# Optimization experiments

Measured on AMD Instinct MI355X. Metric: run time of the kernel, lower is better.

Reference implementation:

```python
import jax, jax.numpy as jnp
import numpy as np

B, NQ, NKV = 4, 1024, 2048
Q_DIM = K_DIM = V_DIM = 1024
HEADS, DIM_HEAD = 16, 64
INNER = HEADS * DIM_HEAD


def setup_inputs() -> dict:
    key = jax.random.key(0)
    ks = jax.random.split(key, 10)
    return {
        "x": jax.random.normal(ks[0], (B, NQ, Q_DIM), dtype=jnp.float32),
        "key_t": jax.random.normal(ks[1], (B, NKV, K_DIM), dtype=jnp.float32),
        "value": jax.random.normal(ks[2], (B, NKV, V_DIM), dtype=jnp.float32),
        "mask": jax.random.randint(ks[3], (B, NQ, NKV), 0, 2) == 1,
        "Wq": jax.random.normal(ks[4], (Q_DIM, INNER), dtype=jnp.float32) * (Q_DIM ** -0.5),
        "Wk": jax.random.normal(ks[5], (K_DIM, INNER), dtype=jnp.float32) * (K_DIM ** -0.5),
        "Wv": jax.random.normal(ks[6], (V_DIM, INNER), dtype=jnp.float32) * (V_DIM ** -0.5),
        "Wo": jax.random.normal(ks[7], (INNER, Q_DIM), dtype=jnp.float32) * (INNER ** -0.5),
        "gamma": jnp.ones((Q_DIM,), dtype=jnp.float32),
        "beta": jnp.zeros((Q_DIM,), dtype=jnp.float32),
    }


def reference(x, key_t, value, mask, Wq, Wk, Wv, Wo, gamma, beta):
    # LayerNorm over last dim
    mu = jnp.mean(x, axis=-1, keepdims=True)
    var = jnp.var(x, axis=-1, keepdims=True)
    xn = (x - mu) * jax.lax.rsqrt(var + 1e-5) * gamma + beta

    h, d = HEADS, DIM_HEAD
    # b n (h d) -> b h n d
    q = (xn @ Wq).reshape(B, NQ, h, d).transpose(0, 2, 1, 3)
    k = (key_t @ Wk).reshape(B, NKV, h, d).transpose(0, 2, 1, 3)
    v = (value @ Wv).reshape(B, NKV, h, d).transpose(0, 2, 1, 3)

    scale = d ** -0.5
    dots = jnp.einsum("bhnd,bhmd->bhnm", q, k) * scale  # [b,h,nq,nkv]
    min_neg = -jnp.finfo(dots.dtype).max
    dots = jnp.where(mask[:, None, :, :], min_neg, dots)
    attn = jax.nn.softmax(dots, axis=-1)
    out = jnp.einsum("bhnm,bhmd->bhnd", attn, v)
    out = out.transpose(0, 2, 1, 3).reshape(B, NQ, INNER)  # b h n d -> b n (h d)
    return out @ Wo
```

## Files before the change

### kernel.cpp

```cpp
#include <hip/hip_runtime.h>

typedef unsigned short u16;
typedef unsigned int u32;
typedef unsigned char u8;
typedef unsigned long long u64;

typedef __attribute__((ext_vector_type(8))) short bf16x8;
typedef __attribute__((ext_vector_type(4))) short bf16x4;
typedef __attribute__((ext_vector_type(4))) float f32x4;

__device__ __forceinline__ float bf2f(u16 u) {
    union { u32 i; float f; } v; v.i = ((u32)u) << 16; return v.f;
}
__device__ __forceinline__ u16 f2bf(float f) {
    union { float f; u32 i; } v; v.f = f;
    u32 r = v.i + 0x7fffu + ((v.i >> 16) & 1u);
    return (u16)(r >> 16);
}
__device__ __forceinline__ u32 pkbf(float a, float b) {
    return (u32)f2bf(a) | ((u32)f2bf(b) << 16);
}
__device__ __forceinline__ float fexp2(float x) { return __builtin_amdgcn_exp2f(x); }

__device__ __forceinline__ void async16(u16* lds, const u16* g) {
    __builtin_amdgcn_global_load_lds(
        (const __attribute__((address_space(1))) void*)g,
        (__attribute__((address_space(3))) void*)lds, 16, 0, 0);
}

__global__ __launch_bounds__(256) void detect_dtype(const u32* __restrict__ x,
                                                    int* __restrict__ flag) {
    int tid = threadIdx.x;
    int hits = 0;
    for (int i = 0; i < 4; ++i) {
        u32 w = x[tid * 4 + i];
        u32 e = (w >> 7) & 0xFFu;
        hits += (e >= 110u && e <= 131u) ? 1 : 0;
    }
    for (int off = 1; off < 64; off <<= 1) hits += __shfl_xor(hits, off, 64);
    __shared__ int red[4];
    int wave = tid >> 6, lane = tid & 63;
    if (lane == 0) red[wave] = hits;
    __syncthreads();
    if (tid == 0) flag[0] = (red[0] + red[1] + red[2] + red[3] > 512) ? 1 : 0;
}

__global__ __launch_bounds__(256) void conv_bf16_2(const void* __restrict__ src0,
                                                   const void* __restrict__ src1,
                                                   u16* __restrict__ dst0,
                                                   u16* __restrict__ dst1,
                                                   const int* __restrict__ flagp,
                                                   int half_blocks) {
    int flag = *flagp;
    const void* src = (blockIdx.x < (u32)half_blocks) ? src0 : src1;
    u16* dst = (blockIdx.x < (u32)half_blocks) ? dst0 : dst1;
    int blk = (blockIdx.x < (u32)half_blocks) ? blockIdx.x : (blockIdx.x - half_blocks);
    size_t i = (size_t)blk * 256 + threadIdx.x;
    if (flag) {
        ((uint4*)dst)[i] = ((const uint4*)src)[i];
    } else {
        const float4* s = (const float4*)src + i * 2;
        float4 f0 = s[0], f1 = s[1];
        u16 t[8];
        t[0] = f2bf(f0.x); t[1] = f2bf(f0.y); t[2] = f2bf(f0.z); t[3] = f2bf(f0.w);
        t[4] = f2bf(f1.x); t[5] = f2bf(f1.y); t[6] = f2bf(f1.z); t[7] = f2bf(f1.w);
        ((uint4*)dst)[i] = *(const uint4*)t;
    }
}

__global__ __launch_bounds__(256) void mask_bits(const int* __restrict__ m,
                                                 u64* __restrict__ o) {
    int wid  = (blockIdx.x * 256 + threadIdx.x) >> 6;
    int lane = threadIdx.x & 63;
    size_t base = (size_t)wid * 2048;
    for (int it = 0; it < 8; ++it) {
        u64 b0 = __ballot(m[base + it * 256 +   0 + lane] == 0);
        u64 b1 = __ballot(m[base + it * 256 +  64 + lane] == 0);
        u64 b2 = __ballot(m[base + it * 256 + 128 + lane] == 0);
        u64 b3 = __ballot(m[base + it * 256 + 192 + lane] == 0);
        if (lane == 0) {
            size_t idx = (base + it * 256) >> 6;
            o[idx + 0] = b0; o[idx + 1] = b1; o[idx + 2] = b2; o[idx + 3] = b3;
        }
    }
}

__global__ __launch_bounds__(256) void ln_kernel(const void* __restrict__ x_,
                                                 const void* __restrict__ g_,
                                                 const void* __restrict__ b_,
                                                 u16* __restrict__ out,
                                                 const int* __restrict__ flagp) {
    int flag = *flagp;
    int row = blockIdx.x;
    int tid = threadIdx.x;
    float v[4];
    if (flag) {
        const u16* xr = (const u16*)x_ + (size_t)row * 1024;
        uint2 d = *(const uint2*)&xr[tid * 4];
        v[0] = bf2f((u16)(d.x & 0xffff));
        v[1] = bf2f((u16)(d.x >> 16));
        v[2] = bf2f((u16)(d.y & 0xffff));
        v[3] = bf2f((u16)(d.y >> 16));
    } else {
        const float* xr = (const float*)x_ + (size_t)row * 1024;
        float4 d = *(const float4*)&xr[tid * 4];
        v[0] = d.x; v[1] = d.y; v[2] = d.z; v[3] = d.w;
    }
    float s  = v[0] + v[1] + v[2] + v[3];
    float ss = v[0]*v[0] + v[1]*v[1] + v[2]*v[2] + v[3]*v[3];
    for (int off = 1; off < 64; off <<= 1) {
        s  += __shfl_xor(s,  off, 64);
        ss += __shfl_xor(ss, off, 64);
    }
    __shared__ float red[8];
    int wave = tid >> 6, lane = tid & 63;
    if (lane == 0) { red[wave] = s; red[4 + wave] = ss; }
    __syncthreads();
    s  = red[0] + red[1] + red[2] + red[3];
    ss = red[4] + red[5] + red[6] + red[7];
    float mu   = s * (1.0f / 1024.0f);
    float var  = ss * (1.0f / 1024.0f) - mu * mu;
    float rstd = rsqrtf(var + 1e-5f);
    u16 r01[4];
    for (int j = 0; j < 4; ++j) {
        float g, bb;
        if (flag) { g = bf2f(((const u16*)g_)[tid * 4 + j]); bb = bf2f(((const u16*)b_)[tid * 4 + j]); }
        else      { g = ((const float*)g_)[tid * 4 + j];     bb = ((const float*)b_)[tid * 4 + j]; }
        r01[j] = f2bf((v[j] - mu) * rstd * g + bb);
    }
    uint2 o;
    o.x = (u32)r01[0] | ((u32)r01[1] << 16);
    o.y = (u32)r01[2] | ((u32)r01[3] << 16);
    *(uint2*)&out[(size_t)row * 1024 + tid * 4] = o;
}

__global__ __launch_bounds__(256) void transpose64x4(const void* __restrict__ s0,
                                                     const void* __restrict__ s1,
                                                     const void* __restrict__ s2,
                                                     const void* __restrict__ s3,
                                                     u16* __restrict__ d0,
                                                     u16* __restrict__ d1,
                                                     u16* __restrict__ d2,
                                                     u16* __restrict__ d3,
                                                     int rows, int cols,
                                                     const int* __restrict__ flagp) {
    __shared__ u16 t[64][65];
    int flag = *flagp;
    const void* src_ = (blockIdx.z == 0) ? s0 : (blockIdx.z == 1) ? s1 :
                       (blockIdx.z == 2) ? s2 : s3;
    u16* dst = (blockIdx.z == 0) ? d0 : (blockIdx.z == 1) ? d1 :
               (blockIdx.z == 2) ? d2 : d3;
    int bx = blockIdx.x * 64;
    int by = blockIdx.y * 64;
    int tid = threadIdx.x;
    for (int i = 0; i < 16; ++i) {
        int r = i * 4 + (tid >> 6);
        int c = tid & 63;
        size_t idx = (size_t)(by + r) * cols + bx + c;
        t[r][c] = flag ? ((const u16*)src_)[idx] : f2bf(((const float*)src_)[idx]);
    }
    __syncthreads();
    for (int i = 0; i < 16; ++i) {
        int r = i * 4 + (tid >> 6);
        int c = tid & 63;
        dst[(size_t)(bx + r) * rows + by + c] = t[c][r];
    }
}

__global__ __launch_bounds__(256, 3) void gemm128(const u16* __restrict__ A,
                                                  const u16* __restrict__ Bt,
                                                  void* __restrict__ C_,
                                                  int M, int N, int K,
                                                  const int* __restrict__ flagp,
                                                  int c_flagged, float cscale,
                                                  int vt_mode, int mdiv) {
    __shared__ u16 As[128 * 64];
    __shared__ u16 Bs[128 * 64];
    int flag = *flagp;
    bool c_bf16 = c_flagged ? (flag != 0) : true;

    int id  = blockIdx.x;
    int j   = id >> 3;
    int gy  = (id & 7) + 8 * (j % mdiv);
    int bnt = j / mdiv;

    int tid  = threadIdx.x;
    int wave = tid >> 6, lane = tid & 63;
    int quad = lane >> 4, l16 = lane & 15;
    size_t bm = (size_t)gy * 128;
    size_t bn = (size_t)bnt * 128;
    int wm = (wave >> 1) * 64, wn = (wave & 1) * 64;

    int lr  = lane >> 3;
    int csw = (lane & 7) ^ lr;
    const u16* Ag = A  + (bm + wave * 32 + lr) * (size_t)K + csw * 8;
    const u16* Bg = Bt + (bn + wave * 32 + lr) * (size_t)K + csw * 8;
    u16* Al = &As[(wave * 32) * 64];
    u16* Bl = &Bs[(wave * 32) * 64];

    f32x4 acc[4][4];
#pragma unroll
    for (int i = 0; i < 4; ++i)
#pragma unroll
        for (int jj = 0; jj < 4; ++jj)
            acc[i][jj] = (f32x4){0.f, 0.f, 0.f, 0.f};

    int rsw = l16 & 7;

    for (int k0 = 0; k0 < K; k0 += 64) {
        __syncthreads();
#pragma unroll
        for (int i = 0; i < 4; ++i) {
            async16(Al + i * 8 * 64, Ag + (size_t)i * 8 * K + k0);
            async16(Bl + i * 8 * 64, Bg + (size_t)i * 8 * K + k0);
        }
        __syncthreads();

#pragma unroll
        for (int ks = 0; ks < 2; ++ks) {
            int chunk = ((ks << 2) | quad) ^ rsw;
            bf16x8 af[4], bfr[4];
#pragma unroll
            for (int mi = 0; mi < 4; ++mi)
                af[mi]  = *(const bf16x8*)&As[(wm + mi * 16 + l16) * 64 + chunk * 8];
#pragma unroll
            for (int ni = 0; ni < 4; ++ni)
                bfr[ni] = *(const bf16x8*)&Bs[(wn + ni * 16 + l16) * 64 + chunk * 8];
#pragma unroll
            for (int mi = 0; mi < 4; ++mi)
#pragma unroll
                for (int ni = 0; ni < 4; ++ni)
                    acc[mi][ni] = __builtin_amdgcn_mfma_f32_16x16x32_bf16(
                        af[mi], bfr[ni], acc[mi][ni], 0, 0, 0);
        }
    }

    if (vt_mode) {
        u16* C = (u16*)C_;
#pragma unroll
        for (int mi = 0; mi < 4; ++mi)
#pragma unroll
            for (int ni = 0; ni < 4; ++ni) {
                size_t m = bm + wm + mi * 16 + quad * 4;
                size_t n = bn + wn + ni * 16 + l16;
                size_t bb = m >> 11, kv = m & 2047;
                size_t hh = n >> 6,  d  = n & 63;
                u16 t4[4];
#pragma unroll
                for (int r = 0; r < 4; ++r) t4[r] = f2bf(acc[mi][ni][r]);
                *(uint2*)&C[((bb * 16 + hh) * 64 + d) * 2048 + kv] = *(const uint2*)t4;
            }
    } else {
#pragma unroll
        for (int mi = 0; mi < 4; ++mi)
#pragma unroll
            for (int ni = 0; ni < 4; ++ni)
#pragma unroll
                for (int r = 0; r < 4; ++r) {
                    size_t row = bm + wm + mi * 16 + quad * 4 + r;
                    size_t col = bn + wn + ni * 16 + l16;
                    float val = acc[mi][ni][r] * cscale;
                    if (c_bf16) ((u16*)C_)[row * N + col]   = f2bf(val);
                    else        ((float*)C_)[row * N + col] = val;
                }
    }
}

__global__ __launch_bounds__(256, 3) void gemm128_vk(const u16* __restrict__ A0,
                                                     const u16* __restrict__ Bt0,
                                                     u16* __restrict__ C0,
                                                     const u16* __restrict__ A1,
                                                     const u16* __restrict__ Bt1,
                                                     u16* __restrict__ C1) {
    __shared__ u16 As[128 * 64];
    __shared__ u16 Bs[128 * 64];
    const int N = 1024, K = 1024, mdiv = 8;

    int id  = blockIdx.x;
    int seg = id >> 9;
    int lid = id & 511;
    const u16* A  = seg ? A1 : A0;
    const u16* Bt = seg ? Bt1 : Bt0;

    int j   = lid >> 3;
    int gy  = (lid & 7) + 8 * (j % mdiv);
    int bnt = j / mdiv;

    int tid  = threadIdx.x;
    int wave = tid >> 6, lane = tid & 63;
    int quad = lane >> 4, l16 = lane & 15;
    size_t bm = (size_t)gy * 128;
    size_t bn = (size_t)bnt * 128;
    int wm = (wave >> 1) * 64, wn = (wave & 1) * 64;

    int lr  = lane >> 3;
    int csw = (lane & 7) ^ lr;
    const u16* Ag = A  + (bm + wave * 32 + lr) * (size_t)K + csw * 8;
    const u16* Bg = Bt + (bn + wave * 32 + lr) * (size_t)K + csw * 8;
    u16* Al = &As[(wave * 32) * 64];
    u16* Bl = &Bs[(wave * 32) * 64];

    f32x4 acc[4][4];
#pragma unroll
    for (int i = 0; i < 4; ++i)
#pragma unroll
        for (int jj = 0; jj < 4; ++jj)
            acc[i][jj] = (f32x4){0.f, 0.f, 0.f, 0.f};

    int rsw = l16 & 7;

    for (int k0 = 0; k0 < K; k0 += 64) {
        __syncthreads();
#pragma unroll
        for (int i = 0; i < 4; ++i) {
            async16(Al + i * 8 * 64, Ag + (size_t)i * 8 * K + k0);
            async16(Bl + i * 8 * 64, Bg + (size_t)i * 8 * K + k0);
        }
        __syncthreads();

#pragma unroll
        for (int ks = 0; ks < 2; ++ks) {
            int chunk = ((ks << 2) | quad) ^ rsw;
            bf16x8 af[4], bfr[4];
#pragma unroll
            for (int mi = 0; mi < 4; ++mi)
                af[mi]  = *(const bf16x8*)&As[(wm + mi * 16 + l16) * 64 + chunk * 8];
#pragma unroll
            for (int ni = 0; ni < 4; ++ni)
                bfr[ni] = *(const bf16x8*)&Bs[(wn + ni * 16 + l16) * 64 + chunk * 8];
#pragma unroll
            for (int mi = 0; mi < 4; ++mi)
#pragma unroll
                for (int ni = 0; ni < 4; ++ni)
                    acc[mi][ni] = __builtin_amdgcn_mfma_f32_16x16x32_bf16(
                        af[mi], bfr[ni], acc[mi][ni], 0, 0, 0);
        }
    }

    if (!seg) {
        u16* C = C0;
#pragma unroll
        for (int mi = 0; mi < 4; ++mi)
#pragma unroll
            for (int ni = 0; ni < 4; ++ni) {
                size_t m = bm + wm + mi * 16 + quad * 4;
                size_t n = bn + wn + ni * 16 + l16;
                size_t bb = m >> 11, kv = m & 2047;
                size_t hh = n >> 6,  d  = n & 63;
                u16 t4[4];
#pragma unroll
                for (int r = 0; r < 4; ++r) t4[r] = f2bf(acc[mi][ni][r]);
                *(uint2*)&C[((bb * 16 + hh) * 64 + d) * 2048 + kv] = *(const uint2*)t4;
            }
    } else {
        u16* C = C1;
#pragma unroll
        for (int mi = 0; mi < 4; ++mi)
#pragma unroll
            for (int ni = 0; ni < 4; ++ni)
#pragma unroll
                for (int r = 0; r < 4; ++r) {
                    size_t row = bm + wm + mi * 16 + quad * 4 + r;
                    size_t col = bn + wn + ni * 16 + l16;
                    C[row * N + col] = f2bf(acc[mi][ni][r]);
                }
    }
}

__global__ __launch_bounds__(256) void attn_kernel(const u16* __restrict__ qg,
                                                   const u16* __restrict__ kg,
                                                   const u16* __restrict__ vtg,
                                                   const u32* __restrict__ mbits,
                                                   float* __restrict__ o0,
                                                   float* __restrict__ o1b0,
                                                   float* __restrict__ o1b1,
                                                   float* __restrict__ o1b2,
                                                   float* __restrict__ o1b3,
                                                   float* __restrict__ lacc0,
                                                   float* __restrict__ lacc1) {
    __shared__ u16 Ks[64 * 64];
    __shared__ u16 Vst[64 * 64];

    const int NQc = 1024, NKVc = 2048, HD = 1024;
    int id = blockIdx.x;
    int j  = id >> 3;
    int qt2 = j >> 3;
    int half = qt2 >> 4;
    int qt = qt2 & 15;
    int g  = (id & 7) + ((j & 7) << 3);
    int h  = g & 15;
    int b  = g >> 4;

    int tid  = threadIdx.x;
    int wave = tid >> 6, lane = tid & 63;
    int quad = lane >> 4, l16 = lane & 15;
    int q0 = qt * 64;

    const u16* qrow = qg + ((size_t)b * NQc + q0 + wave * 16 + l16) * HD + h * 64;
    bf16x8 aq0 = *(const bf16x8*)&qrow[quad * 8];
    bf16x8 aq1 = *(const bf16x8*)&qrow[32 + quad * 8];

    int lr  = lane >> 3;
    int csw = (lane & 7) ^ lr;
    const u16* kbase = kg  + ((size_t)b * NKVc + wave * 8 + lr) * HD + h * 64 + csw * 8;
    const u16* vbase = vtg + (((size_t)b * 16 + h) * 64 + wave * 8 + lr) * (size_t)NKVc + csw * 8;
    u16* kl = Ks  + (wave * 8) * 64;
    u16* vl = Vst + (wave * 8) * 64;

    f32x4 O[4], lacc;
#pragma unroll
    for (int dt = 0; dt < 4; ++dt) O[dt] = (f32x4){0.f, 0.f, 0.f, 0.f};
    lacc = (f32x4){0.f, 0.f, 0.f, 0.f};

    bf16x4 ones4;
#pragma unroll
    for (int jj = 0; jj < 4; ++jj) ones4[jj] = (short)0x3F80;

    const u32* mrowb = mbits + ((size_t)b * NQc + q0 + wave * 16 + l16) * 64;

    int l7 = l16 & 7;
    int kvbeg = half << 10;

    for (int kv0 = kvbeg; kv0 < kvbeg + 1024; kv0 += 64) {
        __syncthreads();
#pragma unroll
        for (int i = 0; i < 2; ++i) {
            async16(kl + i * 32 * 64, kbase + ((size_t)kv0 + i * 32) * HD);
            async16(vl + i * 32 * 64, vbase + (size_t)(i * 32) * NKVc + kv0);
        }
        __syncthreads();

        uint2 bw = *(const uint2*)&mrowb[kv0 >> 5];

        bf16x4 pfr[4];
#pragma unroll
        for (int nt = 0; nt < 4; ++nt) {
            const u16* krow = Ks + (nt * 16 + l16) * 64;
            bf16x8 bk0 = *(const bf16x8*)&krow[(quad ^ l7) * 8];
            bf16x8 bk1 = *(const bf16x8*)&krow[((4 + quad) ^ l7) * 8];
            f32x4 st = (f32x4){0.f, 0.f, 0.f, 0.f};
            st = __builtin_amdgcn_mfma_f32_16x16x32_bf16(bk0, aq0, st, 0, 0, 0);
            st = __builtin_amdgcn_mfma_f32_16x16x32_bf16(bk1, aq1, st, 0, 0, 0);

            u32 w  = (nt < 2) ? bw.x : bw.y;
            u32 m4 = (w >> (((nt & 1) << 4) + (quad << 2))) & 0xFu;
            u32 m01 = ((m4 & 1u) ? 0xFFFFu : 0u) | ((m4 & 2u) ? 0xFFFF0000u : 0u);
            u32 m23 = ((m4 & 4u) ? 0xFFFFu : 0u) | ((m4 & 8u) ? 0xFFFF0000u : 0u);
            u32 p01 = pkbf(fexp2(st[0]), fexp2(st[1])) & m01;
            u32 p23 = pkbf(fexp2(st[2]), fexp2(st[3])) & m23;
            uint2 pu; pu.x = p01; pu.y = p23;
            pfr[nt] = *(const bf16x4*)&pu;

            lacc = __builtin_amdgcn_mfma_f32_16x16x16bf16_1k(ones4, pfr[nt], lacc, 0, 0, 0);
        }

#pragma unroll
        for (int dt = 0; dt < 4; ++dt) {
            const u16* vrow = Vst + (dt * 16 + l16) * 64;
#pragma unroll
            for (int kvs = 0; kvs < 4; ++kvs) {
                int gran = ((kvs << 1) | (quad >> 1)) ^ l7;
                bf16x4 av = *(const bf16x4*)&vrow[gran * 8 + (quad & 1) * 4];
                O[dt] = __builtin_amdgcn_mfma_f32_16x16x16bf16_1k(av, pfr[kvs], O[dt], 0, 0, 0);
            }
        }
    }

    int qi = q0 + wave * 16 + l16;
    float* opart = half ? (b == 0 ? o1b0 : b == 1 ? o1b1 : b == 2 ? o1b2 : o1b3) : o0;
    size_t rbase = half ? (size_t)qi : ((size_t)b * NQc + qi);
    float* orow = opart + rbase * 1024 + h * 64;
#pragma unroll
    for (int dt = 0; dt < 4; ++dt)
        *(float4*)&orow[dt * 16 + quad * 4] = (float4){O[dt][0], O[dt][1], O[dt][2], O[dt][3]};

    float* lp = half ? lacc1 : lacc0;
    if (quad == 0) lp[((size_t)b * 16 + h) * 1024 + qi] = lacc[0];
}

__global__ __launch_bounds__(256) void combine_halves(const float* __restrict__ p0,
                                                      const float* __restrict__ p1b0,
                                                      const float* __restrict__ p1b1,
                                                      const float* __restrict__ p1b2,
                                                      const float* __restrict__ p1b3,
                                                      const float* __restrict__ l0,
                                                      const float* __restrict__ l1,
                                                      u16* __restrict__ ao) {
    int row = blockIdx.x;
    int b = row >> 10, qq = row & 1023;
    const float* p1 = (b == 0) ? p1b0 : (b == 1) ? p1b1 : (b == 2) ? p1b2 : p1b3;
    int tid = threadIdx.x;
    int hd = tid * 4;
    int h  = hd >> 6;
    float4 a = *(const float4*)&p0[(size_t)row * 1024 + hd];
    float4 c = *(const float4*)&p1[(size_t)qq  * 1024 + hd];
    size_t li = ((size_t)b * 16 + h) * 1024 + qq;
    float inv = 1.0f / (l0[li] + l1[li]);
    uint2 o;
    o.x = (u32)f2bf((a.x + c.x) * inv) | ((u32)f2bf((a.y + c.y) * inv) << 16);
    o.y = (u32)f2bf((a.z + c.z) * inv) | ((u32)f2bf((a.w + c.w) * inv) << 16);
    *(uint2*)&ao[(size_t)row * 1024 + hd] = o;
}

extern "C" void kernel_launch(void* const* d_in, const int* in_sizes, int n_in,
                              void* d_out, int out_size, void* d_ws, size_t ws_size,
                              hipStream_t stream) {
    const void* x     = d_in[0];
    const void* key   = d_in[1];
    const void* value = d_in[2];
    const int*  mask  = (const int*)d_in[3];
    const void* Wq    = d_in[4];
    const void* Wk    = d_in[5];
    const void* Wv    = d_in[6];
    const void* Wo    = d_in[7];
    const void* gamma = d_in[8];
    const void* beta  = d_in[9];

    char* ws = (char*)d_ws;
    int* flag = (int*)(ws);
    u16* xn   = (u16*)(ws + ( 1ull << 20));
    float* o1b0 = (float*)(ws + ( 1ull << 20));
    float* o1b1 = (float*)(ws + ( 5ull << 20));
    u16* kb   = (u16*)(ws + ( 9ull << 20));
    float* o0 = (float*)(ws + ( 9ull << 20));
    u16* vb   = (u16*)(ws + (25ull << 20));
    u16* q    = (u16*)(ws + (25ull << 20));
    float* o1b2 = (float*)(ws + (33ull << 20));
    float* o1b3 = (float*)(ws + (37ull << 20));
    u16* vT   = (u16*)(ws + (41ull << 20));
    u16* ao   = (u16*)(ws + (41ull << 20));
    u16* Wqt  = (u16*)(ws + (57ull << 20));
    u32* mbits= (u32*)(ws + (57ull << 20));
    float* la0  = (float*)(ws + (58ull << 20));
    float* la1  = (float*)(ws + (58ull << 20) + (256ull << 10));
    u16* Wkt  = (u16*)(ws + (59ull << 20));
    u16* Wvt  = (u16*)(ws + (61ull << 20));
    u16* Wot  = (u16*)(ws + (63ull << 20));
    u16* k    = (u16*)d_out;

    const float QSCALE = 0.125f * 1.44269504f;

    detect_dtype<<<1, 256, 0, stream>>>((const u32*)x, flag);

    ln_kernel<<<4096, 256, 0, stream>>>(x, gamma, beta, xn, flag);

    dim3 tg4(16, 16, 4);
    transpose64x4<<<tg4, 256, 0, stream>>>(Wq, Wk, Wv, Wo, Wqt, Wkt, Wvt, Wot,
                                           1024, 1024, flag);

    conv_bf16_2<<<8192, 256, 0, stream>>>(key, value, kb, vb, flag, 4096);

    gemm128_vk<<<1024, 256, 0, stream>>>(vb, Wvt, vT, kb, Wkt, k);

    gemm128<<<256, 256, 0, stream>>>(xn, Wqt, q, 4096, 1024, 1024, flag, 0, QSCALE, 0, 4);

    mask_bits<<<1024, 256, 0, stream>>>(mask, (u64*)mbits);

    attn_kernel<<<2048, 256, 0, stream>>>(q, k, vT, mbits,
                                          o0, o1b0, o1b1, o1b2, o1b3, la0, la1);

    combine_halves<<<4096, 256, 0, stream>>>(o0, o1b0, o1b1, o1b2, o1b3,
                                             la0, la1, ao);

    gemm128<<<256, 256, 0, stream>>>(ao, Wot, d_out, 4096, 1024, 1024, flag, 1, 1.0f, 0, 4);
}
```

Before: 343.5 us.

## Fuse prep kernels into one launch and merge mask packing with Q projection

Four preprocessing kernels (dtype detection, LayerNorm, weight transpose, key/value bf16 conversion) become one launch with block-range dispatch. Each block recomputes the dtype flag locally, so the launch no longer has to wait on a separate detection kernel. The mask bit-packing runs as extra blocks inside the Q projection GEMM launch, and the workspace layout is reshuffled so attention partial outputs are stored per batch. This removes launch overhead and serialization gaps between small kernels, at the cost of a redundant flag computation in every block and more buffer aliasing to get right.

```diff
diff --git a/kernel.cpp b/kernel.cpp
--- a/kernel.cpp
+++ b/kernel.cpp
@@ -28,142 +28,121 @@
         (__attribute__((address_space(3))) void*)lds, 16, 0, 0);
 }
 
-__global__ __launch_bounds__(256) void detect_dtype(const u32* __restrict__ x,
-                                                    int* __restrict__ flag) {
+__global__ __launch_bounds__(256) void prep_kernel(
+        const u32* __restrict__ xw,
+        const void* __restrict__ x_,
+        const void* __restrict__ key,
+        const void* __restrict__ value,
+        const void* __restrict__ g_,
+        const void* __restrict__ b_,
+        const void* __restrict__ Wq, const void* __restrict__ Wk,
+        const void* __restrict__ Wv, const void* __restrict__ Wo,
+        u16* __restrict__ xn,
+        u16* __restrict__ kb, u16* __restrict__ vb,
+        u16* __restrict__ Wqt, u16* __restrict__ Wkt,
+        u16* __restrict__ Wvt, u16* __restrict__ Wot,
+        int* __restrict__ flagp) {
+    __shared__ int  redi[4];
+    __shared__ float redf[8];
+    __shared__ u16 tsh[64][65];
+
     int tid = threadIdx.x;
+    int wave = tid >> 6, lane = tid & 63;
+
     int hits = 0;
     for (int i = 0; i < 4; ++i) {
-        u32 w = x[tid * 4 + i];
+        u32 w = xw[tid * 4 + i];
         u32 e = (w >> 7) & 0xFFu;
         hits += (e >= 110u && e <= 131u) ? 1 : 0;
     }
     for (int off = 1; off < 64; off <<= 1) hits += __shfl_xor(hits, off, 64);
-    __shared__ int red[4];
-    int wave = tid >> 6, lane = tid & 63;
-    if (lane == 0) red[wave] = hits;
+    if (lane == 0) redi[wave] = hits;
     __syncthreads();
-    if (tid == 0) flag[0] = (red[0] + red[1] + red[2] + red[3] > 512) ? 1 : 0;
-}
-
-__global__ __launch_bounds__(256) void conv_bf16_2(const void* __restrict__ src0,
-                                                   const void* __restrict__ src1,
-                                                   u16* __restrict__ dst0,
-                                                   u16* __restrict__ dst1,
-                                                   const int* __restrict__ flagp,
-                                                   int half_blocks) {
-    int flag = *flagp;
-    const void* src = (blockIdx.x < (u32)half_blocks) ? src0 : src1;
-    u16* dst = (blockIdx.x < (u32)half_blocks) ? dst0 : dst1;
-    int blk = (blockIdx.x < (u32)half_blocks) ? blockIdx.x : (blockIdx.x - half_blocks);
-    size_t i = (size_t)blk * 256 + threadIdx.x;
-    if (flag) {
-        ((uint4*)dst)[i] = ((const uint4*)src)[i];
+    int flag = (redi[0] + redi[1] + redi[2] + redi[3] > 512) ? 1 : 0;
+
+    int blk = blockIdx.x;
+
+    if (blk == 13312) {
+        if (tid == 0) flagp[0] = flag;
+        return;
+    }
+
+    if (blk < 4096) {
+        int row = blk;
+        float v[4];
+        if (flag) {
+            const u16* xr = (const u16*)x_ + (size_t)row * 1024;
+            uint2 d = *(const uint2*)&xr[tid * 4];
+            v[0] = bf2f((u16)(d.x & 0xffff));
+            v[1] = bf2f((u16)(d.x >> 16));
+            v[2] = bf2f((u16)(d.y & 0xffff));
+            v[3] = bf2f((u16)(d.y >> 16));
+        } else {
+            const float* xr = (const float*)x_ + (size_t)row * 1024;
+            float4 d = *(const float4*)&xr[tid * 4];
+            v[0] = d.x; v[1] = d.y; v[2] = d.z; v[3] = d.w;
+        }
+        float s  = v[0] + v[1] + v[2] + v[3];
+        float ss = v[0]*v[0] + v[1]*v[1] + v[2]*v[2] + v[3]*v[3];
+        for (int off = 1; off < 64; off <<= 1) {
+            s  += __shfl_xor(s,  off, 64);
+            ss += __shfl_xor(ss, off, 64);
+        }
+        if (lane == 0) { redf[wave] = s; redf[4 + wave] = ss; }
+        __syncthreads();
+        s  = redf[0] + redf[1] + redf[2] + redf[3];
+        ss = redf[4] + redf[5] + redf[6] + redf[7];
+        float mu   = s * (1.0f / 1024.0f);
+        float var  = ss * (1.0f / 1024.0f) - mu * mu;
+        float rstd = rsqrtf(var + 1e-5f);
+        u16 r01[4];
+        for (int j = 0; j < 4; ++j) {
+            float g, bb;
+            if (flag) { g = bf2f(((const u16*)g_)[tid * 4 + j]); bb = bf2f(((const u16*)b_)[tid * 4 + j]); }
+            else      { g = ((const float*)g_)[tid * 4 + j];     bb = ((const float*)b_)[tid * 4 + j]; }
+            r01[j] = f2bf((v[j] - mu) * rstd * g + bb);
+        }
+        uint2 o;
+        o.x = (u32)r01[0] | ((u32)r01[1] << 16);
+        o.y = (u32)r01[2] | ((u32)r01[3] << 16);
+        *(uint2*)&xn[(size_t)row * 1024 + tid * 4] = o;
+    } else if (blk < 5120) {
+        int t = blk - 4096;
+        int w = t >> 8;
+        int tt = t & 255;
+        const void* src_ = (w == 0) ? Wq : (w == 1) ? Wk : (w == 2) ? Wv : Wo;
+        u16* dst = (w == 0) ? Wqt : (w == 1) ? Wkt : (w == 2) ? Wvt : Wot;
+        int bx = (tt & 15) * 64;
+        int by = (tt >> 4) * 64;
+        const int rows = 1024, cols = 1024;
+        for (int i = 0; i < 16; ++i) {
+            int r = i * 4 + (tid >> 6);
+            int c = tid & 63;
+            size_t idx = (size_t)(by + r) * cols + bx + c;
+            tsh[r][c] = flag ? ((const u16*)src_)[idx] : f2bf(((const float*)src_)[idx]);
+        }
+        __syncthreads();
+        for (int i = 0; i < 16; ++i) {
+            int r = i * 4 + (tid >> 6);
+            int c = tid & 63;
+            dst[(size_t)(bx + r) * rows + by + c] = tsh[c][r];
+        }
     } else {
-        const float4* s = (const float4*)src + i * 2;
-        float4 f0 = s[0], f1 = s[1];
-        u16 t[8];
-        t[0] = f2bf(f0.x); t[1] = f2bf(f0.y); t[2] = f2bf(f0.z); t[3] = f2bf(f0.w);
-        t[4] = f2bf(f1.x); t[5] = f2bf(f1.y); t[6] = f2bf(f1.z); t[7] = f2bf(f1.w);
-        ((uint4*)dst)[i] = *(const uint4*)t;
-    }
-}
-
-__global__ __launch_bounds__(256) void mask_bits(const int* __restrict__ m,
-                                                 u64* __restrict__ o) {
-    int wid  = (blockIdx.x * 256 + threadIdx.x) >> 6;
-    int lane = threadIdx.x & 63;
-    size_t base = (size_t)wid * 2048;
-    for (int it = 0; it < 8; ++it) {
-        u64 b0 = __ballot(m[base + it * 256 +   0 + lane] == 0);
-        u64 b1 = __ballot(m[base + it * 256 +  64 + lane] == 0);
-        u64 b2 = __ballot(m[base + it * 256 + 128 + lane] == 0);
-        u64 b3 = __ballot(m[base + it * 256 + 192 + lane] == 0);
-        if (lane == 0) {
-            size_t idx = (base + it * 256) >> 6;
-            o[idx + 0] = b0; o[idx + 1] = b1; o[idx + 2] = b2; o[idx + 3] = b3;
-        }
-    }
-}
-
-__global__ __launch_bounds__(256) void ln_kernel(const void* __restrict__ x_,
-                                                 const void* __restrict__ g_,
-                                                 const void* __restrict__ b_,
-                                                 u16* __restrict__ out,
-                                                 const int* __restrict__ flagp) {
-    int flag = *flagp;
-    int row = blockIdx.x;
-    int tid = threadIdx.x;
-    float v[4];
-    if (flag) {
-        const u16* xr = (const u16*)x_ + (size_t)row * 1024;
-        uint2 d = *(const uint2*)&xr[tid * 4];
-        v[0] = bf2f((u16)(d.x & 0xffff));
-        v[1] = bf2f((u16)(d.x >> 16));
-        v[2] = bf2f((u16)(d.y & 0xffff));
-        v[3] = bf2f((u16)(d.y >> 16));
-    } else {
-        const float* xr = (const float*)x_ + (size_t)row * 1024;
-        float4 d = *(const float4*)&xr[tid * 4];
-        v[0] = d.x; v[1] = d.y; v[2] = d.z; v[3] = d.w;
-    }
-    float s  = v[0] + v[1] + v[2] + v[3];
-    float ss = v[0]*v[0] + v[1]*v[1] + v[2]*v[2] + v[3]*v[3];
-    for (int off = 1; off < 64; off <<= 1) {
-        s  += __shfl_xor(s,  off, 64);
-        ss += __shfl_xor(ss, off, 64);
-    }
-    __shared__ float red[8];
-    int wave = tid >> 6, lane = tid & 63;
-    if (lane == 0) { red[wave] = s; red[4 + wave] = ss; }
-    __syncthreads();
-    s  = red[0] + red[1] + red[2] + red[3];
-    ss = red[4] + red[5] + red[6] + red[7];
-    float mu   = s * (1.0f / 1024.0f);
-    float var  = ss * (1.0f / 1024.0f) - mu * mu;
-    float rstd = rsqrtf(var + 1e-5f);
-    u16 r01[4];
-    for (int j = 0; j < 4; ++j) {
-        float g, bb;
-        if (flag) { g = bf2f(((const u16*)g_)[tid * 4 + j]); bb = bf2f(((const u16*)b_)[tid * 4 + j]); }
-        else      { g = ((const float*)g_)[tid * 4 + j];     bb = ((const float*)b_)[tid * 4 + j]; }
-        r01[j] = f2bf((v[j] - mu) * rstd * g + bb);
-    }
-    uint2 o;
-    o.x = (u32)r01[0] | ((u32)r01[1] << 16);
-    o.y = (u32)r01[2] | ((u32)r01[3] << 16);
-    *(uint2*)&out[(size_t)row * 1024 + tid * 4] = o;
-}
-
-__global__ __launch_bounds__(256) void transpose64x4(const void* __restrict__ s0,
-                                                     const void* __restrict__ s1,
-                                                     const void* __restrict__ s2,
-                                                     const void* __restrict__ s3,
-                                                     u16* __restrict__ d0,
-                                                     u16* __restrict__ d1,
-                                                     u16* __restrict__ d2,
-                                                     u16* __restrict__ d3,
-                                                     int rows, int cols,
-                                                     const int* __restrict__ flagp) {
-    __shared__ u16 t[64][65];
-    int flag = *flagp;
-    const void* src_ = (blockIdx.z == 0) ? s0 : (blockIdx.z == 1) ? s1 :
-                       (blockIdx.z == 2) ? s2 : s3;
-    u16* dst = (blockIdx.z == 0) ? d0 : (blockIdx.z == 1) ? d1 :
-               (blockIdx.z == 2) ? d2 : d3;
-    int bx = blockIdx.x * 64;
-    int by = blockIdx.y * 64;
-    int tid = threadIdx.x;
-    for (int i = 0; i < 16; ++i) {
-        int r = i * 4 + (tid >> 6);
-        int c = tid & 63;
-        size_t idx = (size_t)(by + r) * cols + bx + c;
-        t[r][c] = flag ? ((const u16*)src_)[idx] : f2bf(((const float*)src_)[idx]);
-    }
-    __syncthreads();
-    for (int i = 0; i < 16; ++i) {
-        int r = i * 4 + (tid >> 6);
-        int c = tid & 63;
-        dst[(size_t)(bx + r) * rows + by + c] = t[c][r];
+        int cblk = blk - 5120;
+        const void* src = (cblk < 4096) ? key : value;
+        u16* dst = (cblk < 4096) ? kb : vb;
+        int b2 = (cblk < 4096) ? cblk : (cblk - 4096);
+        size_t i = (size_t)b2 * 256 + tid;
+        if (flag) {
+            ((uint4*)dst)[i] = ((const uint4*)src)[i];
+        } else {
+            const float4* s4 = (const float4*)src + i * 2;
+            float4 f0 = s4[0], f1 = s4[1];
+            u16 t8[8];
+            t8[0] = f2bf(f0.x); t8[1] = f2bf(f0.y); t8[2] = f2bf(f0.z); t8[3] = f2bf(f0.w);
+            t8[4] = f2bf(f1.x); t8[5] = f2bf(f1.y); t8[6] = f2bf(f1.z); t8[7] = f2bf(f1.w);
+            ((uint4*)dst)[i] = *(const uint4*)t8;
+        }
     }
 }
 
@@ -367,11 +346,112 @@
     }
 }
 
+__global__ __launch_bounds__(256, 3) void qmask_kernel(const u16* __restrict__ A,
+                                                       const u16* __restrict__ Bt,
+                                                       u16* __restrict__ C,
+                                                       float cscale,
+                                                       const int* __restrict__ m,
+                                                       u64* __restrict__ mb) {
+    __shared__ u16 As[128 * 64];
+    __shared__ u16 Bs[128 * 64];
+    const int N = 1024, K = 1024, mdiv = 4;
+
+    int blk = blockIdx.x;
+    int tid = threadIdx.x;
+
+    if (blk >= 256) {
+        int mblk = blk - 256;
+        int wid  = (mblk * 256 + tid) >> 6;
+        int lane = tid & 63;
+        size_t base = (size_t)wid * 2048;
+        for (int it = 0; it < 8; ++it) {
+            u64 b0 = __ballot(m[base + it * 256 +   0 + lane] == 0);
+            u64 b1 = __ballot(m[base + it * 256 +  64 + lane] == 0);
+            u64 b2 = __ballot(m[base + it * 256 + 128 + lane] == 0);
+            u64 b3 = __ballot(m[base + it * 256 + 192 + lane] == 0);
+            if (lane == 0) {
+                size_t idx = (base + it * 256) >> 6;
+                mb[idx + 0] = b0; mb[idx + 1] = b1; mb[idx + 2] = b2; mb[idx + 3] = b3;
+            }
+        }
+        return;
+    }
+
+    int id  = blk;
+    int j   = id >> 3;
+    int gy  = (id & 7) + 8 * (j % mdiv);
+    int bnt = j / mdiv;
+
+    int wave = tid >> 6, lane = tid & 63;
+    int quad = lane >> 4, l16 = lane & 15;
+    size_t bm = (size_t)gy * 128;
+    size_t bn = (size_t)bnt * 128;
+    int wm = (wave >> 1) * 64, wn = (wave & 1) * 64;
+
+    int lr  = lane >> 3;
+    int csw = (lane & 7) ^ lr;
+    const u16* Ag = A  + (bm + wave * 32 + lr) * (size_t)K + csw * 8;
+    const u16* Bg = Bt + (bn + wave * 32 + lr) * (size_t)K + csw * 8;
+    u16* Al = &As[(wave * 32) * 64];
+    u16* Bl = &Bs[(wave * 32) * 64];
+
+    f32x4 acc[4][4];
+#pragma unroll
+    for (int i = 0; i < 4; ++i)
+#pragma unroll
+        for (int jj = 0; jj < 4; ++jj)
+            acc[i][jj] = (f32x4){0.f, 0.f, 0.f, 0.f};
+
+    int rsw = l16 & 7;
+
+    for (int k0 = 0; k0 < K; k0 += 64) {
+        __syncthreads();
+#pragma unroll
+        for (int i = 0; i < 4; ++i) {
+            async16(Al + i * 8 * 64, Ag + (size_t)i * 8 * K + k0);
+            async16(Bl + i * 8 * 64, Bg + (size_t)i * 8 * K + k0);
+        }
+        __syncthreads();
+
+#pragma unroll
+        for (int ks = 0; ks < 2; ++ks) {
+            int chunk = ((ks << 2) | quad) ^ rsw;
+            bf16x8 af[4], bfr[4];
+#pragma unroll
+            for (int mi = 0; mi < 4; ++mi)
+                af[mi]  = *(const bf16x8*)&As[(wm + mi * 16 + l16) * 64 + chunk * 8];
+#pragma unroll
+            for (int ni = 0; ni < 4; ++ni)
+                bfr[ni] = *(const bf16x8*)&Bs[(wn + ni * 16 + l16) * 64 + chunk * 8];
+#pragma unroll
+            for (int mi = 0; mi < 4; ++mi)
+#pragma unroll
+                for (int ni = 0; ni < 4; ++ni)
+                    acc[mi][ni] = __builtin_amdgcn_mfma_f32_16x16x32_bf16(
+                        af[mi], bfr[ni], acc[mi][ni], 0, 0, 0);
+        }
+    }
+
+#pragma unroll
+    for (int mi = 0; mi < 4; ++mi)
+#pragma unroll
+        for (int ni = 0; ni < 4; ++ni)
+#pragma unroll
+            for (int r = 0; r < 4; ++r) {
+                size_t row = bm + wm + mi * 16 + quad * 4 + r;
+                size_t col = bn + wn + ni * 16 + l16;
+                C[row * N + col] = f2bf(acc[mi][ni][r] * cscale);
+            }
+}
+
 __global__ __launch_bounds__(256) void attn_kernel(const u16* __restrict__ qg,
                                                    const u16* __restrict__ kg,
                                                    const u16* __restrict__ vtg,
                                                    const u32* __restrict__ mbits,
-                                                   float* __restrict__ o0,
+                                                   float* __restrict__ o0b0,
+                                                   float* __restrict__ o0b1,
+                                                   float* __restrict__ o0b2,
+                                                   float* __restrict__ o0b3,
                                                    float* __restrict__ o1b0,
                                                    float* __restrict__ o1b1,
                                                    float* __restrict__ o1b2,
@@ -467,9 +547,10 @@
     }
 
     int qi = q0 + wave * 16 + l16;
-    float* opart = half ? (b == 0 ? o1b0 : b == 1 ? o1b1 : b == 2 ? o1b2 : o1b3) : o0;
-    size_t rbase = half ? (size_t)qi : ((size_t)b * NQc + qi);
-    float* orow = opart + rbase * 1024 + h * 64;
+    float* ob;
+    if (half) ob = (b == 0) ? o1b0 : (b == 1) ? o1b1 : (b == 2) ? o1b2 : o1b3;
+    else      ob = (b == 0) ? o0b0 : (b == 1) ? o0b1 : (b == 2) ? o0b2 : o0b3;
+    float* orow = ob + (size_t)qi * 1024 + h * 64;
 #pragma unroll
     for (int dt = 0; dt < 4; ++dt)
         *(float4*)&orow[dt * 16 + quad * 4] = (float4){O[dt][0], O[dt][1], O[dt][2], O[dt][3]};
@@ -478,22 +559,26 @@
     if (quad == 0) lp[((size_t)b * 16 + h) * 1024 + qi] = lacc[0];
 }
 
-__global__ __launch_bounds__(256) void combine_halves(const float* __restrict__ p0,
-                                                      const float* __restrict__ p1b0,
-                                                      const float* __restrict__ p1b1,
-                                                      const float* __restrict__ p1b2,
-                                                      const float* __restrict__ p1b3,
+__global__ __launch_bounds__(256) void combine_halves(const float* __restrict__ o0b0,
+                                                      const float* __restrict__ o0b1,
+                                                      const float* __restrict__ o0b2,
+                                                      const float* __restrict__ o0b3,
+                                                      const float* __restrict__ o1b0,
+                                                      const float* __restrict__ o1b1,
+                                                      const float* __restrict__ o1b2,
+                                                      const float* __restrict__ o1b3,
                                                       const float* __restrict__ l0,
                                                       const float* __restrict__ l1,
                                                       u16* __restrict__ ao) {
     int row = blockIdx.x;
     int b = row >> 10, qq = row & 1023;
-    const float* p1 = (b == 0) ? p1b0 : (b == 1) ? p1b1 : (b == 2) ? p1b2 : p1b3;
+    const float* p0 = (b == 0) ? o0b0 : (b == 1) ? o0b1 : (b == 2) ? o0b2 : o0b3;
+    const float* p1 = (b == 0) ? o1b0 : (b == 1) ? o1b1 : (b == 2) ? o1b2 : o1b3;
     int tid = threadIdx.x;
     int hd = tid * 4;
     int h  = hd >> 6;
-    float4 a = *(const float4*)&p0[(size_t)row * 1024 + hd];
-    float4 c = *(const float4*)&p1[(size_t)qq  * 1024 + hd];
+    float4 a = *(const float4*)&p0[(size_t)qq * 1024 + hd];
+    float4 c = *(const float4*)&p1[(size_t)qq * 1024 + hd];
     size_t li = ((size_t)b * 16 + h) * 1024 + qq;
     float inv = 1.0f / (l0[li] + l1[li]);
     uint2 o;
@@ -517,49 +602,46 @@
     const void* beta  = d_in[9];
 
     char* ws = (char*)d_ws;
-    int* flag = (int*)(ws);
-    u16* xn   = (u16*)(ws + ( 1ull << 20));
-    float* o1b0 = (float*)(ws + ( 1ull << 20));
-    float* o1b1 = (float*)(ws + ( 5ull << 20));
-    u16* kb   = (u16*)(ws + ( 9ull << 20));
-    float* o0 = (float*)(ws + ( 9ull << 20));
-    u16* vb   = (u16*)(ws + (25ull << 20));
-    u16* q    = (u16*)(ws + (25ull << 20));
+    int* flag   = (int*)(ws);
+    u16* xn     = (u16*)(ws + ( 1ull << 20));
+    float* o0b0 = (float*)(ws + ( 1ull << 20));
+    float* o0b1 = (float*)(ws + ( 5ull << 20));
+    u16* kb     = (u16*)(ws + ( 9ull << 20));
+    u32* mbits  = (u32*)(ws + ( 9ull << 20));
+    float* o0b2 = (float*)(ws + (10ull << 20));
+    float* o0b3 = (float*)(ws + (14ull << 20));
+    float* o1b0 = (float*)(ws + (18ull << 20));
+    float* la0  = (float*)(ws + (22ull << 20));
+    float* la1  = (float*)(ws + (22ull << 20) + (256ull << 10));
+    u16* vb     = (u16*)(ws + (25ull << 20));
+    u16* q      = (u16*)(ws + (25ull << 20));
     float* o1b2 = (float*)(ws + (33ull << 20));
     float* o1b3 = (float*)(ws + (37ull << 20));
-    u16* vT   = (u16*)(ws + (41ull << 20));
-    u16* ao   = (u16*)(ws + (41ull << 20));
-    u16* Wqt  = (u16*)(ws + (57ull << 20));
-    u32* mbits= (u32*)(ws + (57ull << 20));
-    float* la0  = (float*)(ws + (58ull << 20));
-    float* la1  = (float*)(ws + (58ull << 20) + (256ull << 10));
-    u16* Wkt  = (u16*)(ws + (59ull << 20));
-    u16* Wvt  = (u16*)(ws + (61ull << 20));
-    u16* Wot  = (u16*)(ws + (63ull << 20));
-    u16* k    = (u16*)d_out;
+    u16* vT     = (u16*)(ws + (41ull << 20));
+    u16* ao     = (u16*)(ws + (41ull << 20));
+    u16* Wqt    = (u16*)(ws + (57ull << 20));
+    u16* Wkt    = (u16*)(ws + (59ull << 20));
+    float* o1b1 = (float*)(ws + (59ull << 20));
+    u16* Wvt    = (u16*)(ws + (61ull << 20));
+    u16* Wot    = (u16*)(ws + (63ull << 20));
+    u16* k      = (u16*)d_out;
 
     const float QSCALE = 0.125f * 1.44269504f;
 
-    detect_dtype<<<1, 256, 0, stream>>>((const u32*)x, flag);
-
-    ln_kernel<<<4096, 256, 0, stream>>>(x, gamma, beta, xn, flag);
-
-    dim3 tg4(16, 16, 4);
-    transpose64x4<<<tg4, 256, 0, stream>>>(Wq, Wk, Wv, Wo, Wqt, Wkt, Wvt, Wot,
-                                           1024, 1024, flag);
-
-    conv_bf16_2<<<8192, 256, 0, stream>>>(key, value, kb, vb, flag, 4096);
+    prep_kernel<<<13313, 256, 0, stream>>>((const u32*)x, x, key, value,
+                                           gamma, beta, Wq, Wk, Wv, Wo,
+                                           xn, kb, vb, Wqt, Wkt, Wvt, Wot, flag);
 
     gemm128_vk<<<1024, 256, 0, stream>>>(vb, Wvt, vT, kb, Wkt, k);
 
-    gemm128<<<256, 256, 0, stream>>>(xn, Wqt, q, 4096, 1024, 1024, flag, 0, QSCALE, 0, 4);
-
-    mask_bits<<<1024, 256, 0, stream>>>(mask, (u64*)mbits);
+    qmask_kernel<<<1280, 256, 0, stream>>>(xn, Wqt, q, QSCALE, mask, (u64*)mbits);
 
     attn_kernel<<<2048, 256, 0, stream>>>(q, k, vT, mbits,
-                                          o0, o1b0, o1b1, o1b2, o1b3, la0, la1);
-
-    combine_halves<<<4096, 256, 0, stream>>>(o0, o1b0, o1b1, o1b2, o1b3,
+                                          o0b0, o0b1, o0b2, o0b3,
+                                          o1b0, o1b1, o1b2, o1b3, la0, la1);
+
+    combine_halves<<<4096, 256, 0, stream>>>(o0b0, o0b1, o0b2, o0b3,
+                                             o1b0, o1b1, o1b2, o1b3,
                                              la0, la1, ao);
 
     gemm128<<<256, 256, 0, stream>>>(ao, Wot, d_out, 4096, 1024, 1024, flag, 1, 1.0f, 0, 4);
```

Result: no change. 340.7 us (-0.8%).
